# Kernel optimization log

Hardware: AMD Instinct MI355X
Metric: run time of the kernel (lower is better)

Reference implementation:

```python
import jax, jax.numpy as jnp
import numpy as np

BITS = 4            # OPU.bits
VEC = 64            # OPU.input_vector_len / weight_vector_len
QMAX = 2 ** (BITS - 1) - 1   # 7


def ste_round(x):
    # straight-through round (onn_round)
    return x + jax.lax.stop_gradient(jnp.round(x) - x)


@jax.custom_vjp
def onn_dot_sum(x, w):
    # x: [N, R, VEC], w: [VEC, R, M]
    # per-chunk matmul -> clamp to int8 range -> binarize (>=0 -> 1) -> sum over chunks
    s = jnp.einsum('nrc,crm->nrm', x, w)
    s = jnp.clip(s, -128.0, 127.0)
    return jnp.where(s < 0, 0.0, 1.0).sum(axis=1)  # [N, M]


def _onn_dot_fwd(x, w):
    return onn_dot_sum(x, w), (x, w)


def _onn_dot_bwd(res, g):
    # onn_dot_fun.backward: straight-through past clamp+threshold;
    # each chunk receives the same grad g (sum over chunks).
    x, w = res
    gx = jnp.einsum('nm,crm->nrc', g, w)
    gw = jnp.einsum('nrc,nm->crm', x, g)
    return gx, gw


onn_dot_sum.defvjp(_onn_dot_fwd, _onn_dot_bwd)


def _onn_conv2d(inp, weight):
    B, C, H, W = inp.shape
    Cout, Cin, k, _ = weight.shape
    pad = (k - 1) // 2  # SAME, stride=1
    # im2col (matches torch F.unfold channel-major ordering: C, kh, kw)
    xp = jnp.pad(inp, ((0, 0), (0, 0), (pad, pad), (pad, pad)))
    patches = jnp.stack([xp[:, :, i:i + H, j:j + W]
                         for i in range(k) for j in range(k)], axis=2)  # [B,C,k*k,H,W]
    inp_unf = patches.reshape(B, C * k * k, H * W).transpose(0, 2, 1)    # [B,L,D]
    # weight quantization: STE round + clamp to 4-bit signed range
    scale = (2 ** BITS - 1) / (weight.max() - weight.min() + 1e-9)
    wq = jnp.clip(ste_round(weight * scale), -QMAX, QMAX)
    w_ = wq.reshape(Cout, -1).T                                          # [D, Cout]
    D = C * k * k
    repeats = -(-D // VEC)
    padD = VEC * repeats - D
    x = jnp.pad(inp_unf, ((0, 0), (0, 0), (0, padD))).reshape(B * H * W, repeats, VEC)
    wpad = jnp.pad(w_, ((0, padD), (0, 0)))                              # [VEC*R, Cout]
    wr = wpad.T.reshape(Cout, repeats, VEC).transpose(2, 1, 0)           # [VEC,R,Cout]
    temp = onn_dot_sum(x, wr)                                            # [B*L, Cout]
    return temp.reshape(B, H * W, Cout).transpose(0, 2, 1).reshape(B, Cout, H, W)


def setup_inputs() -> dict:
    key = jax.random.key(0)
    k1, k2 = jax.random.split(key)
    B, Cin, H, W = 16, 128, 32, 32
    Cout, k = 256, 3
    inp = jax.random.normal(k1, (B, Cin, H, W), dtype=jnp.float32)
    fan_in = Cin * k * k
    bound = 1.0 / np.sqrt(fan_in)  # kaiming_uniform with a=sqrt(5)
    weight = jax.random.uniform(k2, (Cout, Cin, k, k), dtype=jnp.float32,
                                minval=-bound, maxval=bound)
    return {"inp": inp, "weight": weight}


def reference(inp, weight):
    return _onn_conv2d(inp, weight)
```

## Files before the change

### kernel.cpp

```cpp
#include <hip/hip_runtime.h>


#define TAU 0.03f
#define HITCAP 2048

typedef short short8 __attribute__((ext_vector_type(8)));
typedef float f32x4 __attribute__((ext_vector_type(4)));
typedef unsigned int uv4 __attribute__((ext_vector_type(4)));

__device__ __forceinline__ unsigned short bf16rn(float v) {
    unsigned u = __float_as_uint(v);
    unsigned r = u + 0x7fffu + ((u >> 16) & 1u);
    return (unsigned short)(r >> 16);
}

__global__ __launch_bounds__(256) void k_prep(const float* __restrict__ w,
                                              const float* __restrict__ inp,
                                              float* __restrict__ pmin,
                                              float* __restrict__ pmax,
                                              unsigned* __restrict__ xpk) {
    if (blockIdx.x < 64) {
        int tid = blockIdx.x * 256 + threadIdx.x;
        float vmin = 1e30f, vmax = -1e30f;
        for (int i = tid; i < 294912; i += 64 * 256) {
            float v = w[i];
            vmin = fminf(vmin, v);
            vmax = fmaxf(vmax, v);
        }
        #pragma unroll
        for (int off = 32; off > 0; off >>= 1) {
            vmin = fminf(vmin, __shfl_down(vmin, off, 64));
            vmax = fmaxf(vmax, __shfl_down(vmax, off, 64));
        }
        __shared__ float smin[4], smax[4];
        int wave = threadIdx.x >> 6;
        if ((threadIdx.x & 63) == 0) { smin[wave] = vmin; smax[wave] = vmax; }
        __syncthreads();
        if (threadIdx.x == 0) {
            #pragma unroll
            for (int i = 1; i < 4; i++) {
                vmin = fminf(vmin, smin[i]);
                vmax = fmaxf(vmax, smax[i]);
            }
            pmin[blockIdx.x] = vmin;
            pmax[blockIdx.x] = vmax;
        }
    } else {
        int bc = blockIdx.x - 64;
        const float* src = inp + (size_t)bc * 1024;
        unsigned* dst = xpk + (size_t)bc * 1156;
        #pragma unroll
        for (int i = 0; i < 5; ++i) {
            int idx = threadIdx.x + i * 256;
            if (idx < 1156) {
                int yy = idx / 34, xx = idx - yy * 34;
                float v = 0.0f;
                int ys = yy - 1, xs_ = xx - 1;
                if ((unsigned)ys < 32u && (unsigned)xs_ < 32u) v = src[ys * 32 + xs_];
                unsigned short h = bf16rn(v);
                float hf = __uint_as_float((unsigned)h << 16);
                unsigned short l = bf16rn(v - hf);
                dst[idx] = (unsigned)h | ((unsigned)l << 16);
            }
        }
    }
}

__device__ __forceinline__ float block_scale(const float* pmin, const float* pmax,
                                             float* sca_lds) {
    int t = threadIdx.x;
    if (t < 64) {
        float vmin = pmin[t];
        float vmax = pmax[t];
        #pragma unroll
        for (int off = 32; off > 0; off >>= 1) {
            vmin = fminf(vmin, __shfl_down(vmin, off, 64));
            vmax = fmaxf(vmax, __shfl_down(vmax, off, 64));
        }
        if (t == 0) {
            float tt = __fadd_rn(__fsub_rn(vmax, vmin), 1e-9f);
            *sca_lds = __fdiv_rn(15.0f, tt);
        }
    }
    __syncthreads();
    return *sca_lds;
}

__global__ __launch_bounds__(256) void k_quantb(const float* __restrict__ w,
                                                const float* __restrict__ pmin,
                                                const float* __restrict__ pmax,
                                                uv4* __restrict__ wqb) {
    __shared__ float sca;
    float s = block_scale(pmin, pmax, &sca);
    int slot = blockIdx.x * 256 + threadIdx.x;
    int lane = slot & 63;
    int sub = slot >> 6;
    int khalf = sub & 1;
    int mt = (sub >> 1) & 3;
    int gr = sub >> 3;
    int g = gr / 18, r = gr - g * 18;
    int m = g * 64 + mt * 16 + (lane & 15);
    int dbase = r * 64 + khalf * 32 + (lane >> 4) * 8;
    const float* wp = w + (size_t)m * 1152 + dbase;
    unsigned o[4];
    #pragma unroll
    for (int p = 0; p < 4; ++p) {
        float q0 = rintf(__fmul_rn(wp[2 * p], s));
        float q1 = rintf(__fmul_rn(wp[2 * p + 1], s));
        q0 = fminf(fmaxf(q0, -7.0f), 7.0f);
        q1 = fminf(fmaxf(q1, -7.0f), 7.0f);
        o[p] = (unsigned)bf16rn(q0) | ((unsigned)bf16rn(q1) << 16);
    }
    uv4 v; v.x = o[0]; v.y = o[1]; v.z = o[2]; v.w = o[3];
    wqb[slot] = v;
}

__global__ __launch_bounds__(256) void k_main(const unsigned* __restrict__ xpk,
                                              const uv4* __restrict__ wqb,
                                              const float* __restrict__ inp,
                                              const float* __restrict__ weight,
                                              const float* __restrict__ pmin,
                                              const float* __restrict__ pmax,
                                              float* __restrict__ out) {
    __shared__ int ofs_s[1152];
    __shared__ unsigned hitbuf[HITCAP];
    __shared__ unsigned hitcnt;
    __shared__ float sca;

    const int t = threadIdx.x;
    if (t == 0) hitcnt = 0u;
    float sc = block_scale(pmin, pmax, &sca);
    for (int k = t; k < 1152; k += 256) {
        int cin = k / 9;
        int rem = k - cin * 9;
        int kh = rem / 3;
        int kw = rem - kh * 3;
        ofs_s[k] = cin * 1156 + kh * 34 + kw;
    }
    __syncthreads();

    const int lane = t & 63;
    const int wv = t >> 6;
    const int quad = lane >> 4;
    const int nl = lane & 15;
    const int n0 = blockIdx.x * 64;
    const int g = blockIdx.y;
    const int b = n0 >> 10;

    const int sy_w = ((n0 & 1023) >> 5) + (wv >> 1);
    const int col0 = (wv & 1) * 16;
    const unsigned* __restrict__ xw =
        xpk + (size_t)b * (128 * 1156) + sy_w * 34 + col0 + nl;
    const uv4* __restrict__ aw = wqb + (size_t)g * (18 * 512) + lane;

    int counts[4][4] = {};

    unsigned pb[16];
    #pragma unroll
    for (int q2 = 0; q2 < 16; ++q2) {
        int k = (q2 >> 3) * 32 + quad * 8 + (q2 & 7);
        pb[q2] = xw[ofs_s[k]];
    }

    for (int r = 0; r < 18; ++r) {
        unsigned cb[16];
        #pragma unroll
        for (int q2 = 0; q2 < 16; ++q2) cb[q2] = pb[q2];
        if (r < 17) {
            #pragma unroll
            for (int q2 = 0; q2 < 16; ++q2) {
                int k = (r + 1) * 64 + (q2 >> 3) * 32 + quad * 8 + (q2 & 7);
                pb[q2] = xw[ofs_s[k]];
            }
        }

        short8 bhi[2], blo[2];
        #pragma unroll
        for (int kh2 = 0; kh2 < 2; ++kh2) {
            union { unsigned d[4]; short8 v; } H, L;
            #pragma unroll
            for (int p = 0; p < 4; ++p) {
                unsigned ua = cb[kh2 * 8 + 2 * p], ub = cb[kh2 * 8 + 2 * p + 1];
                H.d[p] = (ua & 0xffffu) | (ub << 16);
                L.d[p] = (ua >> 16) | (ub & 0xffff0000u);
            }
            bhi[kh2] = H.v;
            blo[kh2] = L.v;
        }

        #pragma unroll
        for (int mt = 0; mt < 4; ++mt) {
            short8 af0 = __builtin_bit_cast(short8, aw[r * 512 + (mt * 2 + 0) * 64]);
            short8 af1 = __builtin_bit_cast(short8, aw[r * 512 + (mt * 2 + 1) * 64]);
            f32x4 acc = {0.0f, 0.0f, 0.0f, 0.0f};
            acc = __builtin_amdgcn_mfma_f32_16x16x32_bf16(af0, bhi[0], acc, 0, 0, 0);
            acc = __builtin_amdgcn_mfma_f32_16x16x32_bf16(af1, bhi[1], acc, 0, 0, 0);
            acc = __builtin_amdgcn_mfma_f32_16x16x32_bf16(af0, blo[0], acc, 0, 0, 0);
            acc = __builtin_amdgcn_mfma_f32_16x16x32_bf16(af1, blo[1], acc, 0, 0, 0);
            #pragma unroll
            for (int i = 0; i < 4; ++i) {
                float s = acc[i];
                int ge = (s >= 0.0f) ? 1 : 0;
                counts[mt][i] += ge;
                if (__builtin_fabsf(s) < TAU) {
                    unsigned idx = atomicAdd(&hitcnt, 1u);
                    if (idx < (unsigned)HITCAP) {
                        unsigned m = (unsigned)(g * 64 + mt * 16 + quad * 4 + i);
                        unsigned n = (unsigned)(n0 + wv * 16 + nl);
                        hitbuf[idx] = n | ((unsigned)r << 14) | (m << 19) | ((unsigned)ge << 27);
                    }
                }
            }
        }
    }

    {
        const int n = n0 + wv * 16 + nl;
        const int p = n & 1023;
        #pragma unroll
        for (int mt = 0; mt < 4; ++mt)
            #pragma unroll
            for (int i = 0; i < 4; ++i) {
                int m = g * 64 + mt * 16 + quad * 4 + i;
                out[(((size_t)(b * 256 + m)) << 10) + p] = (float)counts[mt][i];
            }
    }

    __syncthreads();
    unsigned tot = hitcnt;
    if (tot > (unsigned)HITCAP) tot = (unsigned)HITCAP;
    for (unsigned i = t; i < tot; i += 256) {
        unsigned u = hitbuf[i];
        int n = u & 16383;
        int r = (u >> 14) & 31;
        int m = (u >> 19) & 255;
        int bit = (u >> 27) & 1;
        int bb = n >> 10, p = n & 1023, y = p >> 5, x = p & 31;
        const float* ib = inp + (size_t)bb * (128 * 32 * 32);
        const float* wp = weight + (size_t)m * 1152;
        float s = 0.0f;
        int d = r * 64;
        for (int c = 0; c < 64; ++c, ++d) {
            int ci = d / 9, rem = d - ci * 9;
            int kh = rem / 3, kw = rem - kh * 3;
            int yy = y + kh - 1, xx = x + kw - 1;
            float xv = 0.0f;
            if ((unsigned)yy < 32u && (unsigned)xx < 32u)
                xv = ib[(ci * 32 + yy) * 32 + xx];
            float q = rintf(__fmul_rn(wp[d], sc));
            q = fminf(fmaxf(q, -7.0f), 7.0f);
            s = __fadd_rn(s, __fmul_rn(xv, q));
        }
        int nb = (s >= 0.0f) ? 1 : 0;
        if (nb != bit)
            atomicAdd(&out[(((size_t)(bb * 256 + m)) << 10) + p], nb ? 1.0f : -1.0f);
    }
}

extern "C" void kernel_launch(void* const* d_in, const int* in_sizes, int n_in,
                              void* d_out, int out_size, void* d_ws, size_t ws_size,
                              hipStream_t stream) {
    const float* inp    = (const float*)d_in[0];
    const float* weight = (const float*)d_in[1];
    float* out = (float*)d_out;

    char* ws = (char*)d_ws;
    float*    pmin  = (float*)(ws + 0);
    float*    pmax  = (float*)(ws + 256);
    uv4*      wqb   = (uv4*)(ws + 1024);
    unsigned* xpk   = (unsigned*)(ws + 590848);

    k_prep<<<2112, 256, 0, stream>>>(weight, inp, pmin, pmax, xpk);
    k_quantb<<<144, 256, 0, stream>>>(weight, pmin, pmax, wqb);

    dim3 grid(256, 4);
    k_main<<<grid, 256, 0, stream>>>(xpk, wqb, inp, weight, pmin, pmax, out);
}
```

Measured before the change: 130.8 us.

## Split chunk loop across two grid slices with atomic accumulation and prefetching

The 18-chunk reduction in the main kernel is split across a new grid z-dimension of 2, doubling the block count so more waves are resident. Counts are now accumulated into the output with atomic adds, and the prep kernel gains extra blocks that zero the output first. The change also software-prefetches the next weight fragments, loads im2col offsets as int4 vectors, uses byte-permute instructions to split the hi/lo halves, and sets a minimum-occupancy launch bound. In exchange it adds output zeroing traffic and atomic contention on the output.

```diff
diff --git a/kernel.cpp b/kernel.cpp
--- a/kernel.cpp
+++ b/kernel.cpp
@@ -18,7 +18,8 @@
                                               const float* __restrict__ inp,
                                               float* __restrict__ pmin,
                                               float* __restrict__ pmax,
-                                              unsigned* __restrict__ xpk) {
+                                              unsigned* __restrict__ xpk,
+                                              float* __restrict__ out) {
     if (blockIdx.x < 64) {
         int tid = blockIdx.x * 256 + threadIdx.x;
         float vmin = 1e30f, vmax = -1e30f;
@@ -45,7 +46,7 @@
             pmin[blockIdx.x] = vmin;
             pmax[blockIdx.x] = vmax;
         }
-    } else {
+    } else if (blockIdx.x < 2112) {
         int bc = blockIdx.x - 64;
         const float* src = inp + (size_t)bc * 1024;
         unsigned* dst = xpk + (size_t)bc * 1156;
@@ -63,6 +64,13 @@
                 dst[idx] = (unsigned)h | ((unsigned)l << 16);
             }
         }
+    } else {
+        int zb = blockIdx.x - 2112;
+        float4* o4 = (float4*)out;
+        float4 z = make_float4(0.0f, 0.0f, 0.0f, 0.0f);
+        int base = zb * 512 + threadIdx.x;
+        o4[base] = z;
+        o4[base + 256] = z;
     }
 }
 
@@ -115,14 +123,25 @@
     wqb[slot] = v;
 }
 
-__global__ __launch_bounds__(256) void k_main(const unsigned* __restrict__ xpk,
-                                              const uv4* __restrict__ wqb,
-                                              const float* __restrict__ inp,
-                                              const float* __restrict__ weight,
-                                              const float* __restrict__ pmin,
-                                              const float* __restrict__ pmax,
-                                              float* __restrict__ out) {
-    __shared__ int ofs_s[1152];
+#define ISSUE_B(rr, dst) do {                                                  \
+    const int4* _oa = reinterpret_cast<const int4*>(&ofs_s[(rr) * 64 + quad * 8]); \
+    int4 _o0 = _oa[0], _o1 = _oa[1];                                           \
+    const int4* _ob = reinterpret_cast<const int4*>(&ofs_s[(rr) * 64 + 32 + quad * 8]); \
+    int4 _o2 = _ob[0], _o3 = _ob[1];                                           \
+    dst[0] = xw[_o0.x]; dst[1] = xw[_o0.y]; dst[2] = xw[_o0.z]; dst[3] = xw[_o0.w]; \
+    dst[4] = xw[_o1.x]; dst[5] = xw[_o1.y]; dst[6] = xw[_o1.z]; dst[7] = xw[_o1.w]; \
+    dst[8] = xw[_o2.x]; dst[9] = xw[_o2.y]; dst[10] = xw[_o2.z]; dst[11] = xw[_o2.w]; \
+    dst[12] = xw[_o3.x]; dst[13] = xw[_o3.y]; dst[14] = xw[_o3.z]; dst[15] = xw[_o3.w]; \
+} while (0)
+
+__global__ __launch_bounds__(256, 6) void k_main(const unsigned* __restrict__ xpk,
+                                                 const uv4* __restrict__ wqb,
+                                                 const float* __restrict__ inp,
+                                                 const float* __restrict__ weight,
+                                                 const float* __restrict__ pmin,
+                                                 const float* __restrict__ pmax,
+                                                 float* __restrict__ out) {
+    __shared__ alignas(16) int ofs_s[1152];
     __shared__ unsigned hitbuf[HITCAP];
     __shared__ unsigned hitcnt;
     __shared__ float sca;
@@ -145,6 +164,8 @@
     const int nl = lane & 15;
     const int n0 = blockIdx.x * 64;
     const int g = blockIdx.y;
+    const int kz = blockIdx.z;
+    const int r0 = kz * 9, rend = r0 + 9;
     const int b = n0 >> 10;
 
     const int sy_w = ((n0 & 1023) >> 5) + (wv >> 1);
@@ -156,23 +177,15 @@
     int counts[4][4] = {};
 
     unsigned pb[16];
-    #pragma unroll
-    for (int q2 = 0; q2 < 16; ++q2) {
-        int k = (q2 >> 3) * 32 + quad * 8 + (q2 & 7);
-        pb[q2] = xw[ofs_s[k]];
-    }
-
-    for (int r = 0; r < 18; ++r) {
+    ISSUE_B(r0, pb);
+    short8 ac0 = __builtin_bit_cast(short8, aw[r0 * 512]);
+    short8 ac1 = __builtin_bit_cast(short8, aw[r0 * 512 + 64]);
+
+    for (int r = r0; r < rend; ++r) {
         unsigned cb[16];
         #pragma unroll
         for (int q2 = 0; q2 < 16; ++q2) cb[q2] = pb[q2];
-        if (r < 17) {
-            #pragma unroll
-            for (int q2 = 0; q2 < 16; ++q2) {
-                int k = (r + 1) * 64 + (q2 >> 3) * 32 + quad * 8 + (q2 & 7);
-                pb[q2] = xw[ofs_s[k]];
-            }
-        }
+        if (r + 1 < rend) ISSUE_B(r + 1, pb);
 
         short8 bhi[2], blo[2];
         #pragma unroll
@@ -181,8 +194,8 @@
             #pragma unroll
             for (int p = 0; p < 4; ++p) {
                 unsigned ua = cb[kh2 * 8 + 2 * p], ub = cb[kh2 * 8 + 2 * p + 1];
-                H.d[p] = (ua & 0xffffu) | (ub << 16);
-                L.d[p] = (ua >> 16) | (ub & 0xffff0000u);
+                H.d[p] = __builtin_amdgcn_perm(ub, ua, 0x05040100u);
+                L.d[p] = __builtin_amdgcn_perm(ub, ua, 0x07060302u);
             }
             bhi[kh2] = H.v;
             blo[kh2] = L.v;
@@ -190,13 +203,16 @@
 
         #pragma unroll
         for (int mt = 0; mt < 4; ++mt) {
-            short8 af0 = __builtin_bit_cast(short8, aw[r * 512 + (mt * 2 + 0) * 64]);
-            short8 af1 = __builtin_bit_cast(short8, aw[r * 512 + (mt * 2 + 1) * 64]);
+            int pn = (mt == 3) ? (((r + 1) < rend ? (r + 1) : r0) * 512)
+                               : (r * 512 + (mt + 1) * 128);
+            short8 an0 = __builtin_bit_cast(short8, aw[pn]);
+            short8 an1 = __builtin_bit_cast(short8, aw[pn + 64]);
+
             f32x4 acc = {0.0f, 0.0f, 0.0f, 0.0f};
-            acc = __builtin_amdgcn_mfma_f32_16x16x32_bf16(af0, bhi[0], acc, 0, 0, 0);
-            acc = __builtin_amdgcn_mfma_f32_16x16x32_bf16(af1, bhi[1], acc, 0, 0, 0);
-            acc = __builtin_amdgcn_mfma_f32_16x16x32_bf16(af0, blo[0], acc, 0, 0, 0);
-            acc = __builtin_amdgcn_mfma_f32_16x16x32_bf16(af1, blo[1], acc, 0, 0, 0);
+            acc = __builtin_amdgcn_mfma_f32_16x16x32_bf16(ac0, bhi[0], acc, 0, 0, 0);
+            acc = __builtin_amdgcn_mfma_f32_16x16x32_bf16(ac1, bhi[1], acc, 0, 0, 0);
+            acc = __builtin_amdgcn_mfma_f32_16x16x32_bf16(ac0, blo[0], acc, 0, 0, 0);
+            acc = __builtin_amdgcn_mfma_f32_16x16x32_bf16(ac1, blo[1], acc, 0, 0, 0);
             #pragma unroll
             for (int i = 0; i < 4; ++i) {
                 float s = acc[i];
@@ -211,6 +227,8 @@
                     }
                 }
             }
+            ac0 = an0;
+            ac1 = an1;
         }
     }
 
@@ -222,7 +240,8 @@
             #pragma unroll
             for (int i = 0; i < 4; ++i) {
                 int m = g * 64 + mt * 16 + quad * 4 + i;
-                out[(((size_t)(b * 256 + m)) << 10) + p] = (float)counts[mt][i];
+                atomicAdd(&out[(((size_t)(b * 256 + m)) << 10) + p],
+                          (float)counts[mt][i]);
             }
     }
 
@@ -270,9 +289,9 @@
     uv4*      wqb   = (uv4*)(ws + 1024);
     unsigned* xpk   = (unsigned*)(ws + 590848);
 
-    k_prep<<<2112, 256, 0, stream>>>(weight, inp, pmin, pmax, xpk);
+    k_prep<<<4160, 256, 0, stream>>>(weight, inp, pmin, pmax, xpk, out);
     k_quantb<<<144, 256, 0, stream>>>(weight, pmin, pmax, wqb);
 
-    dim3 grid(256, 4);
+    dim3 grid(256, 4, 2);
     k_main<<<grid, 256, 0, stream>>>(xpk, wqb, inp, weight, pmin, pmax, out);
 }
```

Measured after the change: 169.4 us. 29.5% more time.
